# Performance work log

Hardware: AMD Instinct MI355X
Metric: run time of the kernel (lower is better)

Reference implementation:

```python
import jax, jax.numpy as jnp
import numpy as np

EMB_DIM = 128
WEIGHT_COL = 24

def setup_inputs() -> dict:
    key = jax.random.key(0)
    ks = jax.random.split(key, 9)
    B, S = 8, 4096
    s_in = 1.0 / np.sqrt(EMB_DIM)
    s_out = 1.0 / np.sqrt(WEIGHT_COL)
    return {
        "x": jax.random.normal(ks[0], (B, S, EMB_DIM), dtype=jnp.float32),
        "wQ": jax.random.uniform(ks[1], (EMB_DIM, WEIGHT_COL), jnp.float32, -s_in, s_in),
        "bQ": jax.random.uniform(ks[2], (WEIGHT_COL,), jnp.float32, -s_in, s_in),
        "wK": jax.random.uniform(ks[3], (EMB_DIM, WEIGHT_COL), jnp.float32, -s_in, s_in),
        "bK": jax.random.uniform(ks[4], (WEIGHT_COL,), jnp.float32, -s_in, s_in),
        "wV": jax.random.uniform(ks[5], (EMB_DIM, WEIGHT_COL), jnp.float32, -s_in, s_in),
        "bV": jax.random.uniform(ks[6], (WEIGHT_COL,), jnp.float32, -s_in, s_in),
        "wO": jax.random.uniform(ks[7], (WEIGHT_COL, EMB_DIM), jnp.float32, -s_out, s_out),
        "bO": jax.random.uniform(ks[8], (EMB_DIM,), jnp.float32, -s_out, s_out),
    }

def reference(x, wQ, bQ, wK, bK, wV, bV, wO, bO):
    # projections: [B,S,E] -> [B,S,D]
    Q = x @ wQ + bQ
    K = x @ wK + bK
    V = x @ wV + bV
    # NOTE: source scales by sqrt(emb_dim), not sqrt(weight_col)
    scale = 1.0 / np.sqrt(EMB_DIM).astype(np.float32)
    scores = jnp.einsum('bqd,bkd->bqk', Q, K) * scale  # [B,S,S]
    A = jax.nn.softmax(scores, axis=-1)
    H = jnp.einsum('bqk,bkd->bqd', A, V)               # [B,S,D]
    return H @ wO + bO                                  # [B,S,E]
```

## Files before the change

kernel.cpp:

```cpp
#include <hip/hip_runtime.h>


#define B_ 8
#define S_ 4096
#define E_ 128
#define D_ 24
#define N_ (B_ * S_)
#define SCALE 0.08838834764831845f
#define LOG2E 1.4426950408889634f

#define TK 128
#define KS_STRIDE 40
#define VS_STRIDE 136
#define HS_STRIDE 40
#define XS_STRIDE 136
#define OS_STRIDE 84

typedef __attribute__((ext_vector_type(8))) short bfrag;
typedef __attribute__((ext_vector_type(4))) float ffrag;

__device__ inline unsigned short f2bf(float f) {
    unsigned int x = __builtin_bit_cast(unsigned int, f);
    return (unsigned short)((x + 0x7fffu + ((x >> 16) & 1u)) >> 16);
}
__device__ inline unsigned int pack2(float a, float b) {
    return (unsigned int)f2bf(a) | ((unsigned int)f2bf(b) << 16);
}
__device__ inline unsigned int pack2h(float a, float b) {
    unsigned int ua = __builtin_bit_cast(unsigned int, a) + 0x8000u;
    unsigned int ub = __builtin_bit_cast(unsigned int, b) + 0x8000u;
    return __builtin_amdgcn_perm(ub, ua, 0x07060302);
}

__global__ __launch_bounds__(256) void prep_kernel(
    const float* __restrict__ wQ, const float* __restrict__ bQ,
    const float* __restrict__ wK, const float* __restrict__ bK,
    const float* __restrict__ wV, const float* __restrict__ bV,
    const float* __restrict__ wO,
    unsigned short* __restrict__ Wf, unsigned short* __restrict__ wOf,
    float* __restrict__ bqkv)
{
    const int gtid   = blockIdx.x * 256 + threadIdx.x;
    const int stride = gridDim.x * 256;
    const float qs = SCALE * LOG2E;
    for (int idx = gtid; idx < 4 * 5 * 512; idx += stride) {
        const int j    = idx & 7;
        const int lane = (idx >> 3) & 63;
        const int nt   = (idx >> 9) % 5;
        const int kt   = idx / 2560;
        const int n = nt * 16 + (lane & 15);
        const int k = kt * 32 + ((lane >> 4) << 3) + j;
        float v = 0.0f;
        if (n < 24)      v = wQ[k * 24 + n] * qs;
        else if (n < 48) v = wK[k * 24 + (n - 24)];
        else if (n < 72) v = wV[k * 24 + (n - 48)];
        Wf[idx] = f2bf(v);
    }
    for (int idx = gtid; idx < 8 * 512; idx += stride) {
        const int j    = idx & 7;
        const int lane = (idx >> 3) & 63;
        const int nt   = idx >> 9;
        const int k = ((lane >> 4) << 3) + j;
        const int e = nt * 16 + (lane & 15);
        wOf[idx] = (k < 24) ? f2bf(wO[k * 128 + e]) : (unsigned short)0;
    }
    if (gtid < 80) {
        float v = 0.0f;
        if (gtid < 24)      v = bQ[gtid] * qs;
        else if (gtid < 48) v = bK[gtid - 24];
        else if (gtid < 72) v = bV[gtid - 48];
        bqkv[gtid] = v;
    }
}

__global__ __launch_bounds__(256) void proj_kernel(
    const float* __restrict__ x, const unsigned short* __restrict__ Wf,
    const float* __restrict__ bqkv,
    unsigned short* __restrict__ Qbf, unsigned short* __restrict__ Kbf,
    unsigned short* __restrict__ Vt)
{
    __shared__ float smem[64 * OS_STRIDE];
    unsigned short* xs = (unsigned short*)smem;
    float* os = smem;

    const int tid  = threadIdx.x;
    const int lane = tid & 63;
    const int w    = tid >> 6;
    const int col  = lane & 15;
    const int quad = lane >> 4;
    const int rb   = blockIdx.x * 64;

    #pragma unroll
    for (int i = 0; i < 8; ++i) {
        const int idx = i * 256 + tid;
        const int row = idx >> 5, c4 = idx & 31;
        const float4 xv = *(const float4*)(x + (size_t)(rb + row) * 128 + c4 * 4);
        uint2 h;
        h.x = pack2(xv.x, xv.y);
        h.y = pack2(xv.z, xv.w);
        *(uint2*)(&xs[row * XS_STRIDE + c4 * 4]) = h;
    }

    bfrag Wfr[20];
    #pragma unroll
    for (int f = 0; f < 20; ++f)
        Wfr[f] = *(const bfrag*)(Wf + (f * 64 + lane) * 8);

    __syncthreads();

    ffrag acc[5];
    #pragma unroll
    for (int nt = 0; nt < 5; ++nt) acc[nt] = (ffrag){0.f, 0.f, 0.f, 0.f};

    #pragma unroll
    for (int kt = 0; kt < 4; ++kt) {
        const bfrag Af = *(const bfrag*)(&xs[(w * 16 + col) * XS_STRIDE + kt * 32 + quad * 8]);
        #pragma unroll
        for (int nt = 0; nt < 5; ++nt)
            acc[nt] = __builtin_amdgcn_mfma_f32_16x16x32_bf16(Af, Wfr[kt * 5 + nt], acc[nt], 0, 0, 0);
    }

    __syncthreads();

    #pragma unroll
    for (int nt = 0; nt < 5; ++nt) {
        const float bb = bqkv[nt * 16 + col];
        #pragma unroll
        for (int r = 0; r < 4; ++r)
            os[(w * 16 + quad * 4 + r) * OS_STRIDE + nt * 16 + col] = acc[nt][r] + bb;
    }
    __syncthreads();

    {
        const int half  = tid & 1;
        const int row   = (tid >> 1) & 63;
        const int isK   = tid >> 7;
        const int cbase = isK * 24;
        unsigned int pk[8];
        #pragma unroll
        for (int g = 0; g < 8; ++g) {
            const int c0 = half * 16 + g * 2;
            const float f0 = (c0     < 24) ? os[row * OS_STRIDE + cbase + c0]     : 0.0f;
            const float f1 = (c0 + 1 < 24) ? os[row * OS_STRIDE + cbase + c0 + 1] : 0.0f;
            pk[g] = pack2(f0, f1);
        }
        unsigned short* dst = (isK ? Kbf : Qbf) + (size_t)(rb + row) * 32 + half * 16;
        *(uint4*)(dst)     = make_uint4(pk[0], pk[1], pk[2], pk[3]);
        *(uint4*)(dst + 8) = make_uint4(pk[4], pk[5], pk[6], pk[7]);
    }

    if (tid < 192) {
        const int d  = tid % 24;
        const int ch = tid / 24;
        unsigned int p[4];
        #pragma unroll
        for (int g = 0; g < 4; ++g) {
            const float f0 = os[(ch * 8 + g * 2 + 0) * OS_STRIDE + 48 + d];
            const float f1 = os[(ch * 8 + g * 2 + 1) * OS_STRIDE + 48 + d];
            p[g] = pack2(f0, f1);
        }
        const int b = rb >> 12, s0 = rb & 4095;
        uint4* dst = (uint4*)(Vt + (((size_t)(b * 24 + d)) << 12) + s0 + ch * 8);
        *dst = make_uint4(p[0], p[1], p[2], p[3]);
    }
}

__global__ __launch_bounds__(256, 8) void attn_kernel(
    const unsigned short* __restrict__ Qbf, const unsigned short* __restrict__ Kbf,
    const unsigned short* __restrict__ Vt,
    float* __restrict__ Opart, float* __restrict__ lpart)
{
    __shared__ unsigned short Ks[TK * KS_STRIDE];
    __shared__ unsigned short Vs[32 * VS_STRIDE];

    const int tid    = threadIdx.x;
    const int lane   = tid & 63;
    const int w      = tid >> 6;
    const int col    = lane & 15;
    const int quad   = lane >> 4;
    const int blk    = blockIdx.x;
    const int split  = blockIdx.y;
    const int nsp    = gridDim.y;
    const int kchunk = S_ / nsp;
    const int b      = blk >> 6;
    const int qbase  = blk * 64 + w * 16;

    if (tid < 16)
        *(uint4*)(&Vs[24 * VS_STRIDE + tid * 8]) =
            make_uint4(0x3F803F80u, 0x3F803F80u, 0x3F803F80u, 0x3F803F80u);

    const bfrag Qf = *(const bfrag*)(Qbf + (size_t)(qbase + col) * 32 + quad * 8);

    ffrag Ot0 = {0.f, 0.f, 0.f, 0.f};
    ffrag Ot1 = {0.f, 0.f, 0.f, 0.f};

    const unsigned short* Kbase = Kbf + ((size_t)(b * 4096) + split * kchunk) * 32;
    const unsigned short* Vbase = Vt + (size_t)(b * 24) * 4096 + split * kchunk;

    __syncthreads();

    for (int kb = 0; kb < kchunk; kb += TK) {
        #pragma unroll
        for (int i = 0; i < 2; ++i) {
            const int idx = i * 256 + tid;
            const int key = idx >> 2, ch = idx & 3;
            const uint4 t4 = *(const uint4*)(Kbase + (size_t)(kb + key) * 32 + ch * 8);
            const int row = (key & ~31) + (((key >> 2) & 1) << 4)
                          + (((key & 31) >> 3) << 2) + (key & 3);
            *(uint4*)(&Ks[row * KS_STRIDE + ch * 8]) = t4;
        }
        #pragma unroll
        for (int i = 0; i < 2; ++i) {
            const int u = i * 256 + tid;
            if (u < 384) {
                const int d = u >> 4, ch = u & 15;
                const uint4 t4 = *(const uint4*)(Vbase + (size_t)d * 4096 + kb + ch * 8);
                *(uint4*)(&Vs[d * VS_STRIDE + ch * 8]) = t4;
            }
        }
        __syncthreads();

        #pragma unroll
        for (int c2 = 0; c2 < 4; ++c2) {
            const bfrag Kfe = *(const bfrag*)(&Ks[(c2 * 32 + col) * KS_STRIDE + quad * 8]);
            const bfrag Kfo = *(const bfrag*)(&Ks[(c2 * 32 + 16 + col) * KS_STRIDE + quad * 8]);
            ffrag Se = {0.f, 0.f, 0.f, 0.f};
            ffrag So = {0.f, 0.f, 0.f, 0.f};
            Se = __builtin_amdgcn_mfma_f32_16x16x32_bf16(Kfe, Qf, Se, 0, 0, 0);
            So = __builtin_amdgcn_mfma_f32_16x16x32_bf16(Kfo, Qf, So, 0, 0, 0);
            const float pe0 = __builtin_amdgcn_exp2f(Se[0]);
            const float pe1 = __builtin_amdgcn_exp2f(Se[1]);
            const float pe2 = __builtin_amdgcn_exp2f(Se[2]);
            const float pe3 = __builtin_amdgcn_exp2f(Se[3]);
            const float po0 = __builtin_amdgcn_exp2f(So[0]);
            const float po1 = __builtin_amdgcn_exp2f(So[1]);
            const float po2 = __builtin_amdgcn_exp2f(So[2]);
            const float po3 = __builtin_amdgcn_exp2f(So[3]);
            union { bfrag f; unsigned int u[4]; } P;
            P.u[0] = pack2h(pe0, pe1);
            P.u[1] = pack2h(pe2, pe3);
            P.u[2] = pack2h(po0, po1);
            P.u[3] = pack2h(po2, po3);
            const bfrag Va0 = *(const bfrag*)(&Vs[col * VS_STRIDE + c2 * 32 + quad * 8]);
            const bfrag Va1 = *(const bfrag*)(&Vs[(16 + col) * VS_STRIDE + c2 * 32 + quad * 8]);
            Ot0 = __builtin_amdgcn_mfma_f32_16x16x32_bf16(Va0, P.f, Ot0, 0, 0, 0);
            Ot1 = __builtin_amdgcn_mfma_f32_16x16x32_bf16(Va1, P.f, Ot1, 0, 0, 0);
        }
        __syncthreads();
    }

    const size_t base = ((size_t)split * N_ + qbase + col) * 32;
    *(ffrag*)(&Opart[base + quad * 4]) = Ot0;
    if (quad < 2)
        *(ffrag*)(&Opart[base + 16 + quad * 4]) = Ot1;
    if (quad == 2)
        lpart[(size_t)split * N_ + qbase + col] = Ot1[0];
}

__global__ __launch_bounds__(256) void combine_kernel(
    const float* __restrict__ Opart, const float* __restrict__ lpart,
    const unsigned short* __restrict__ wOf, const float* __restrict__ bO,
    float* __restrict__ out, int nsp)
{
    __shared__ unsigned short Hs[64 * HS_STRIDE];

    const int tid = threadIdx.x;
    const int qb  = blockIdx.x * 64;
    {
        const int ql = tid >> 2;
        const int c8 = (tid & 3) * 8;
        const int q  = qb + ql;
        float a[8] = {0.f, 0.f, 0.f, 0.f, 0.f, 0.f, 0.f, 0.f};
        if (c8 < 24) {
            for (int s = 0; s < nsp; ++s) {
                const float* p = &Opart[((size_t)s * N_ + q) * 32 + c8];
                const float4 u = *(const float4*)p;
                const float4 v = *(const float4*)(p + 4);
                a[0] += u.x; a[1] += u.y; a[2] += u.z; a[3] += u.w;
                a[4] += v.x; a[5] += v.y; a[6] += v.z; a[7] += v.w;
            }
        }
        float ls = 0.f;
        for (int s = 0; s < nsp; ++s) ls += lpart[(size_t)s * N_ + q];
        const float inv = 1.0f / ls;
        uint4 pk;
        pk.x = pack2(a[0] * inv, a[1] * inv);
        pk.y = pack2(a[2] * inv, a[3] * inv);
        pk.z = pack2(a[4] * inv, a[5] * inv);
        pk.w = pack2(a[6] * inv, a[7] * inv);
        *(uint4*)(&Hs[ql * HS_STRIDE + c8]) = pk;
    }
    __syncthreads();

    const int lane = tid & 63;
    const int w    = tid >> 6;
    const int col  = lane & 15;
    const int quad = lane >> 4;
    const bfrag Hf = *(const bfrag*)(&Hs[(w * 16 + col) * HS_STRIDE + quad * 8]);
    #pragma unroll
    for (int nt = 0; nt < 8; ++nt) {
        const bfrag Wo = *(const bfrag*)(wOf + (nt * 64 + lane) * 8);
        ffrag C = {0.f, 0.f, 0.f, 0.f};
        C = __builtin_amdgcn_mfma_f32_16x16x32_bf16(Hf, Wo, C, 0, 0, 0);
        const float bo = bO[nt * 16 + col];
        #pragma unroll
        for (int r = 0; r < 4; ++r)
            out[(size_t)(qb + w * 16 + quad * 4 + r) * 128 + nt * 16 + col] = C[r] + bo;
    }
}

extern "C" void kernel_launch(void* const* d_in, const int* in_sizes, int n_in,
                              void* d_out, int out_size, void* d_ws, size_t ws_size,
                              hipStream_t stream) {
    const float* x  = (const float*)d_in[0];
    const float* wQ = (const float*)d_in[1];
    const float* bQ = (const float*)d_in[2];
    const float* wK = (const float*)d_in[3];
    const float* bK = (const float*)d_in[4];
    const float* wV = (const float*)d_in[5];
    const float* bV = (const float*)d_in[6];
    const float* wO = (const float*)d_in[7];
    const float* bO = (const float*)d_in[8];
    float* out = (float*)d_out;

    unsigned short* ws16 = (unsigned short*)d_ws;
    unsigned short* Qbf = ws16;
    unsigned short* Kbf = Qbf + (size_t)N_ * 32;
    unsigned short* Vt  = Kbf + (size_t)N_ * 32;
    unsigned short* Wf  = Vt + (size_t)B_ * 24 * S_;
    unsigned short* wOf = Wf + 4 * 5 * 512;
    float* bqkv = (float*)(wOf + 8 * 512);
    float* Opart = bqkv + 80;
    const size_t baseBytes = (size_t)((char*)Opart - (char*)d_ws);

    int nsp = 4;
    while (nsp > 1) {
        const size_t need = baseBytes + (size_t)nsp * N_ * 32 * 4 + (size_t)nsp * N_ * 4;
        if (need <= ws_size) break;
        nsp >>= 1;
    }
    float* lpart = Opart + (size_t)nsp * N_ * 32;

    prep_kernel<<<8, 256, 0, stream>>>(wQ, bQ, wK, bK, wV, bV, wO, Wf, wOf, bqkv);
    proj_kernel<<<N_ / 64, 256, 0, stream>>>(x, Wf, bqkv, Qbf, Kbf, Vt);
    attn_kernel<<<dim3(N_ / 64, nsp), 256, 0, stream>>>(Qbf, Kbf, Vt, Opart, lpart);
    combine_kernel<<<N_ / 64, 256, 0, stream>>>(Opart, lpart, wOf, bO, out, nsp);
}
```

Before: 125.1 us.

## Process two query tiles per wave in attention kernel to reuse K/V tiles

Each wave now handles two 16-row query tiles (128 queries per block instead of 64), so every K and V fragment loaded from shared memory feeds twice as many MFMAs. The grid halves and launch bounds drop to 4 blocks per CU to allow for the doubled accumulator and score registers. This cuts the global-to-LDS staging of K/V per query and the LDS fragment reads, but lowers occupancy and halves the number of blocks available to spread across CUs.

```diff
diff --git a/kernel.cpp b/kernel.cpp
--- a/kernel.cpp
+++ b/kernel.cpp
@@ -165,7 +165,7 @@
     }
 }
 
-__global__ __launch_bounds__(256, 8) void attn_kernel(
+__global__ __launch_bounds__(256, 4) void attn_kernel(
     const unsigned short* __restrict__ Qbf, const unsigned short* __restrict__ Kbf,
     const unsigned short* __restrict__ Vt,
     float* __restrict__ Opart, float* __restrict__ lpart)
@@ -182,17 +182,21 @@
     const int split  = blockIdx.y;
     const int nsp    = gridDim.y;
     const int kchunk = S_ / nsp;
-    const int b      = blk >> 6;
-    const int qbase  = blk * 64 + w * 16;
+    const int b      = blk >> 5;
+    const int qbase0 = blk * 128 + w * 16;
+    const int qbase1 = qbase0 + 64;
 
     if (tid < 16)
         *(uint4*)(&Vs[24 * VS_STRIDE + tid * 8]) =
             make_uint4(0x3F803F80u, 0x3F803F80u, 0x3F803F80u, 0x3F803F80u);
 
-    const bfrag Qf = *(const bfrag*)(Qbf + (size_t)(qbase + col) * 32 + quad * 8);
-
-    ffrag Ot0 = {0.f, 0.f, 0.f, 0.f};
-    ffrag Ot1 = {0.f, 0.f, 0.f, 0.f};
+    const bfrag Qf0 = *(const bfrag*)(Qbf + (size_t)(qbase0 + col) * 32 + quad * 8);
+    const bfrag Qf1 = *(const bfrag*)(Qbf + (size_t)(qbase1 + col) * 32 + quad * 8);
+
+    ffrag Ot00 = {0.f, 0.f, 0.f, 0.f};
+    ffrag Ot10 = {0.f, 0.f, 0.f, 0.f};
+    ffrag Ot01 = {0.f, 0.f, 0.f, 0.f};
+    ffrag Ot11 = {0.f, 0.f, 0.f, 0.f};
 
     const unsigned short* Kbase = Kbf + ((size_t)(b * 4096) + split * kchunk) * 32;
     const unsigned short* Vbase = Vt + (size_t)(b * 24) * 4096 + split * kchunk;
@@ -224,37 +228,47 @@
         for (int c2 = 0; c2 < 4; ++c2) {
             const bfrag Kfe = *(const bfrag*)(&Ks[(c2 * 32 + col) * KS_STRIDE + quad * 8]);
             const bfrag Kfo = *(const bfrag*)(&Ks[(c2 * 32 + 16 + col) * KS_STRIDE + quad * 8]);
-            ffrag Se = {0.f, 0.f, 0.f, 0.f};
-            ffrag So = {0.f, 0.f, 0.f, 0.f};
-            Se = __builtin_amdgcn_mfma_f32_16x16x32_bf16(Kfe, Qf, Se, 0, 0, 0);
-            So = __builtin_amdgcn_mfma_f32_16x16x32_bf16(Kfo, Qf, So, 0, 0, 0);
-            const float pe0 = __builtin_amdgcn_exp2f(Se[0]);
-            const float pe1 = __builtin_amdgcn_exp2f(Se[1]);
-            const float pe2 = __builtin_amdgcn_exp2f(Se[2]);
-            const float pe3 = __builtin_amdgcn_exp2f(Se[3]);
-            const float po0 = __builtin_amdgcn_exp2f(So[0]);
-            const float po1 = __builtin_amdgcn_exp2f(So[1]);
-            const float po2 = __builtin_amdgcn_exp2f(So[2]);
-            const float po3 = __builtin_amdgcn_exp2f(So[3]);
-            union { bfrag f; unsigned int u[4]; } P;
-            P.u[0] = pack2h(pe0, pe1);
-            P.u[1] = pack2h(pe2, pe3);
-            P.u[2] = pack2h(po0, po1);
-            P.u[3] = pack2h(po2, po3);
+            ffrag Se0 = {0.f, 0.f, 0.f, 0.f};
+            ffrag So0 = {0.f, 0.f, 0.f, 0.f};
+            ffrag Se1 = {0.f, 0.f, 0.f, 0.f};
+            ffrag So1 = {0.f, 0.f, 0.f, 0.f};
+            Se0 = __builtin_amdgcn_mfma_f32_16x16x32_bf16(Kfe, Qf0, Se0, 0, 0, 0);
+            So0 = __builtin_amdgcn_mfma_f32_16x16x32_bf16(Kfo, Qf0, So0, 0, 0, 0);
+            Se1 = __builtin_amdgcn_mfma_f32_16x16x32_bf16(Kfe, Qf1, Se1, 0, 0, 0);
+            So1 = __builtin_amdgcn_mfma_f32_16x16x32_bf16(Kfo, Qf1, So1, 0, 0, 0);
+
+            union { bfrag f; unsigned int u[4]; } P0, P1;
+            P0.u[0] = pack2h(__builtin_amdgcn_exp2f(Se0[0]), __builtin_amdgcn_exp2f(Se0[1]));
+            P0.u[1] = pack2h(__builtin_amdgcn_exp2f(Se0[2]), __builtin_amdgcn_exp2f(Se0[3]));
+            P0.u[2] = pack2h(__builtin_amdgcn_exp2f(So0[0]), __builtin_amdgcn_exp2f(So0[1]));
+            P0.u[3] = pack2h(__builtin_amdgcn_exp2f(So0[2]), __builtin_amdgcn_exp2f(So0[3]));
+            P1.u[0] = pack2h(__builtin_amdgcn_exp2f(Se1[0]), __builtin_amdgcn_exp2f(Se1[1]));
+            P1.u[1] = pack2h(__builtin_amdgcn_exp2f(Se1[2]), __builtin_amdgcn_exp2f(Se1[3]));
+            P1.u[2] = pack2h(__builtin_amdgcn_exp2f(So1[0]), __builtin_amdgcn_exp2f(So1[1]));
+            P1.u[3] = pack2h(__builtin_amdgcn_exp2f(So1[2]), __builtin_amdgcn_exp2f(So1[3]));
+
             const bfrag Va0 = *(const bfrag*)(&Vs[col * VS_STRIDE + c2 * 32 + quad * 8]);
             const bfrag Va1 = *(const bfrag*)(&Vs[(16 + col) * VS_STRIDE + c2 * 32 + quad * 8]);
-            Ot0 = __builtin_amdgcn_mfma_f32_16x16x32_bf16(Va0, P.f, Ot0, 0, 0, 0);
-            Ot1 = __builtin_amdgcn_mfma_f32_16x16x32_bf16(Va1, P.f, Ot1, 0, 0, 0);
+            Ot00 = __builtin_amdgcn_mfma_f32_16x16x32_bf16(Va0, P0.f, Ot00, 0, 0, 0);
+            Ot10 = __builtin_amdgcn_mfma_f32_16x16x32_bf16(Va1, P0.f, Ot10, 0, 0, 0);
+            Ot01 = __builtin_amdgcn_mfma_f32_16x16x32_bf16(Va0, P1.f, Ot01, 0, 0, 0);
+            Ot11 = __builtin_amdgcn_mfma_f32_16x16x32_bf16(Va1, P1.f, Ot11, 0, 0, 0);
         }
         __syncthreads();
     }
 
-    const size_t base = ((size_t)split * N_ + qbase + col) * 32;
-    *(ffrag*)(&Opart[base + quad * 4]) = Ot0;
-    if (quad < 2)
-        *(ffrag*)(&Opart[base + 16 + quad * 4]) = Ot1;
-    if (quad == 2)
-        lpart[(size_t)split * N_ + qbase + col] = Ot1[0];
+    const size_t base0 = ((size_t)split * N_ + qbase0 + col) * 32;
+    const size_t base1 = ((size_t)split * N_ + qbase1 + col) * 32;
+    *(ffrag*)(&Opart[base0 + quad * 4]) = Ot00;
+    *(ffrag*)(&Opart[base1 + quad * 4]) = Ot01;
+    if (quad < 2) {
+        *(ffrag*)(&Opart[base0 + 16 + quad * 4]) = Ot10;
+        *(ffrag*)(&Opart[base1 + 16 + quad * 4]) = Ot11;
+    }
+    if (quad == 2) {
+        lpart[(size_t)split * N_ + qbase0 + col] = Ot10[0];
+        lpart[(size_t)split * N_ + qbase1 + col] = Ot11[0];
+    }
 }
 
 __global__ __launch_bounds__(256) void combine_kernel(
@@ -343,6 +357,6 @@
 
     prep_kernel<<<8, 256, 0, stream>>>(wQ, bQ, wK, bK, wV, bV, wO, Wf, wOf, bqkv);
     proj_kernel<<<N_ / 64, 256, 0, stream>>>(x, Wf, bqkv, Qbf, Kbf, Vt);
-    attn_kernel<<<dim3(N_ / 64, nsp), 256, 0, stream>>>(Qbf, Kbf, Vt, Opart, lpart);
+    attn_kernel<<<dim3(N_ / 128, nsp), 256, 0, stream>>>(Qbf, Kbf, Vt, Opart, lpart);
     combine_kernel<<<N_ / 64, 256, 0, stream>>>(Opart, lpart, wOf, bO, out, nsp);
 }
```

Result: no change. 125.2 us (+0.1%).

## Use 512-thread attention blocks, fp16 partial outputs, and cheaper bf16 packing

Applied to the files above, without the earlier changes.

Attention blocks now have 512 threads covering 128 queries, so each K/V tile staged in shared memory serves twice as many query rows. The partial output accumulators go to the workspace as fp16 instead of fp32, which halves the write and read traffic between the attention and combine kernels. The round-to-nearest-even bf16 packing is replaced by the cheaper add-and-permute packing in the projection and combine kernels. Risks are lower precision in the partial outputs, a possible fp16 overflow on large unnormalized sums, and reduced occupancy from the larger blocks.

```diff
diff --git a/kernel.cpp b/kernel.cpp
--- a/kernel.cpp
+++ b/kernel.cpp
@@ -1,4 +1,5 @@
 #include <hip/hip_runtime.h>
+#include <hip/hip_fp16.h>
 
 
 #define B_ 8
@@ -23,13 +24,13 @@
     unsigned int x = __builtin_bit_cast(unsigned int, f);
     return (unsigned short)((x + 0x7fffu + ((x >> 16) & 1u)) >> 16);
 }
-__device__ inline unsigned int pack2(float a, float b) {
-    return (unsigned int)f2bf(a) | ((unsigned int)f2bf(b) << 16);
-}
 __device__ inline unsigned int pack2h(float a, float b) {
     unsigned int ua = __builtin_bit_cast(unsigned int, a) + 0x8000u;
     unsigned int ub = __builtin_bit_cast(unsigned int, b) + 0x8000u;
     return __builtin_amdgcn_perm(ub, ua, 0x07060302);
+}
+__device__ inline unsigned int packh16(float a, float b) {
+    return __builtin_bit_cast(unsigned int, __builtin_amdgcn_cvt_pkrtz(a, b));
 }
 
 __global__ __launch_bounds__(256) void prep_kernel(
@@ -96,8 +97,8 @@
         const int row = idx >> 5, c4 = idx & 31;
         const float4 xv = *(const float4*)(x + (size_t)(rb + row) * 128 + c4 * 4);
         uint2 h;
-        h.x = pack2(xv.x, xv.y);
-        h.y = pack2(xv.z, xv.w);
+        h.x = pack2h(xv.x, xv.y);
+        h.y = pack2h(xv.z, xv.w);
         *(uint2*)(&xs[row * XS_STRIDE + c4 * 4]) = h;
     }
 
@@ -142,7 +143,7 @@
             const int c0 = half * 16 + g * 2;
             const float f0 = (c0     < 24) ? os[row * OS_STRIDE + cbase + c0]     : 0.0f;
             const float f1 = (c0 + 1 < 24) ? os[row * OS_STRIDE + cbase + c0 + 1] : 0.0f;
-            pk[g] = pack2(f0, f1);
+            pk[g] = pack2h(f0, f1);
         }
         unsigned short* dst = (isK ? Kbf : Qbf) + (size_t)(rb + row) * 32 + half * 16;
         *(uint4*)(dst)     = make_uint4(pk[0], pk[1], pk[2], pk[3]);
@@ -157,7 +158,7 @@
         for (int g = 0; g < 4; ++g) {
             const float f0 = os[(ch * 8 + g * 2 + 0) * OS_STRIDE + 48 + d];
             const float f1 = os[(ch * 8 + g * 2 + 1) * OS_STRIDE + 48 + d];
-            p[g] = pack2(f0, f1);
+            p[g] = pack2h(f0, f1);
         }
         const int b = rb >> 12, s0 = rb & 4095;
         uint4* dst = (uint4*)(Vt + (((size_t)(b * 24 + d)) << 12) + s0 + ch * 8);
@@ -165,10 +166,10 @@
     }
 }
 
-__global__ __launch_bounds__(256, 8) void attn_kernel(
+__global__ __launch_bounds__(512, 8) void attn_kernel(
     const unsigned short* __restrict__ Qbf, const unsigned short* __restrict__ Kbf,
     const unsigned short* __restrict__ Vt,
-    float* __restrict__ Opart, float* __restrict__ lpart)
+    __half* __restrict__ Opart, float* __restrict__ lpart)
 {
     __shared__ unsigned short Ks[TK * KS_STRIDE];
     __shared__ unsigned short Vs[32 * VS_STRIDE];
@@ -182,8 +183,8 @@
     const int split  = blockIdx.y;
     const int nsp    = gridDim.y;
     const int kchunk = S_ / nsp;
-    const int b      = blk >> 6;
-    const int qbase  = blk * 64 + w * 16;
+    const int b      = blk >> 5;
+    const int qbase  = blk * 128 + w * 16;
 
     if (tid < 16)
         *(uint4*)(&Vs[24 * VS_STRIDE + tid * 8]) =
@@ -200,23 +201,17 @@
     __syncthreads();
 
     for (int kb = 0; kb < kchunk; kb += TK) {
-        #pragma unroll
-        for (int i = 0; i < 2; ++i) {
-            const int idx = i * 256 + tid;
-            const int key = idx >> 2, ch = idx & 3;
+        {
+            const int key = tid >> 2, ch = tid & 3;
             const uint4 t4 = *(const uint4*)(Kbase + (size_t)(kb + key) * 32 + ch * 8);
             const int row = (key & ~31) + (((key >> 2) & 1) << 4)
                           + (((key & 31) >> 3) << 2) + (key & 3);
             *(uint4*)(&Ks[row * KS_STRIDE + ch * 8]) = t4;
         }
-        #pragma unroll
-        for (int i = 0; i < 2; ++i) {
-            const int u = i * 256 + tid;
-            if (u < 384) {
-                const int d = u >> 4, ch = u & 15;
-                const uint4 t4 = *(const uint4*)(Vbase + (size_t)d * 4096 + kb + ch * 8);
-                *(uint4*)(&Vs[d * VS_STRIDE + ch * 8]) = t4;
-            }
+        if (tid < 384) {
+            const int d = tid >> 4, ch = tid & 15;
+            const uint4 t4 = *(const uint4*)(Vbase + (size_t)d * 4096 + kb + ch * 8);
+            *(uint4*)(&Vs[d * VS_STRIDE + ch * 8]) = t4;
         }
         __syncthreads();
 
@@ -228,19 +223,11 @@
             ffrag So = {0.f, 0.f, 0.f, 0.f};
             Se = __builtin_amdgcn_mfma_f32_16x16x32_bf16(Kfe, Qf, Se, 0, 0, 0);
             So = __builtin_amdgcn_mfma_f32_16x16x32_bf16(Kfo, Qf, So, 0, 0, 0);
-            const float pe0 = __builtin_amdgcn_exp2f(Se[0]);
-            const float pe1 = __builtin_amdgcn_exp2f(Se[1]);
-            const float pe2 = __builtin_amdgcn_exp2f(Se[2]);
-            const float pe3 = __builtin_amdgcn_exp2f(Se[3]);
-            const float po0 = __builtin_amdgcn_exp2f(So[0]);
-            const float po1 = __builtin_amdgcn_exp2f(So[1]);
-            const float po2 = __builtin_amdgcn_exp2f(So[2]);
-            const float po3 = __builtin_amdgcn_exp2f(So[3]);
             union { bfrag f; unsigned int u[4]; } P;
-            P.u[0] = pack2h(pe0, pe1);
-            P.u[1] = pack2h(pe2, pe3);
-            P.u[2] = pack2h(po0, po1);
-            P.u[3] = pack2h(po2, po3);
+            P.u[0] = pack2h(__builtin_amdgcn_exp2f(Se[0]), __builtin_amdgcn_exp2f(Se[1]));
+            P.u[1] = pack2h(__builtin_amdgcn_exp2f(Se[2]), __builtin_amdgcn_exp2f(Se[3]));
+            P.u[2] = pack2h(__builtin_amdgcn_exp2f(So[0]), __builtin_amdgcn_exp2f(So[1]));
+            P.u[3] = pack2h(__builtin_amdgcn_exp2f(So[2]), __builtin_amdgcn_exp2f(So[3]));
             const bfrag Va0 = *(const bfrag*)(&Vs[col * VS_STRIDE + c2 * 32 + quad * 8]);
             const bfrag Va1 = *(const bfrag*)(&Vs[(16 + col) * VS_STRIDE + c2 * 32 + quad * 8]);
             Ot0 = __builtin_amdgcn_mfma_f32_16x16x32_bf16(Va0, P.f, Ot0, 0, 0, 0);
@@ -250,15 +237,24 @@
     }
 
     const size_t base = ((size_t)split * N_ + qbase + col) * 32;
-    *(ffrag*)(&Opart[base + quad * 4]) = Ot0;
-    if (quad < 2)
-        *(ffrag*)(&Opart[base + 16 + quad * 4]) = Ot1;
+    {
+        uint2 s0;
+        s0.x = packh16(Ot0[0], Ot0[1]);
+        s0.y = packh16(Ot0[2], Ot0[3]);
+        *(uint2*)(Opart + base + quad * 4) = s0;
+    }
+    if (quad < 2) {
+        uint2 s1;
+        s1.x = packh16(Ot1[0], Ot1[1]);
+        s1.y = packh16(Ot1[2], Ot1[3]);
+        *(uint2*)(Opart + base + 16 + quad * 4) = s1;
+    }
     if (quad == 2)
         lpart[(size_t)split * N_ + qbase + col] = Ot1[0];
 }
 
 __global__ __launch_bounds__(256) void combine_kernel(
-    const float* __restrict__ Opart, const float* __restrict__ lpart,
+    const __half* __restrict__ Opart, const float* __restrict__ lpart,
     const unsigned short* __restrict__ wOf, const float* __restrict__ bO,
     float* __restrict__ out, int nsp)
 {
@@ -273,21 +269,23 @@
         float a[8] = {0.f, 0.f, 0.f, 0.f, 0.f, 0.f, 0.f, 0.f};
         if (c8 < 24) {
             for (int s = 0; s < nsp; ++s) {
-                const float* p = &Opart[((size_t)s * N_ + q) * 32 + c8];
-                const float4 u = *(const float4*)p;
-                const float4 v = *(const float4*)(p + 4);
-                a[0] += u.x; a[1] += u.y; a[2] += u.z; a[3] += u.w;
-                a[4] += v.x; a[5] += v.y; a[6] += v.z; a[7] += v.w;
+                const __half2* p2 = (const __half2*)(Opart + ((size_t)s * N_ + q) * 32 + c8);
+                #pragma unroll
+                for (int j = 0; j < 4; ++j) {
+                    const float2 f = __half22float2(p2[j]);
+                    a[2 * j]     += f.x;
+                    a[2 * j + 1] += f.y;
+                }
             }
         }
         float ls = 0.f;
         for (int s = 0; s < nsp; ++s) ls += lpart[(size_t)s * N_ + q];
         const float inv = 1.0f / ls;
         uint4 pk;
-        pk.x = pack2(a[0] * inv, a[1] * inv);
-        pk.y = pack2(a[2] * inv, a[3] * inv);
-        pk.z = pack2(a[4] * inv, a[5] * inv);
-        pk.w = pack2(a[6] * inv, a[7] * inv);
+        pk.x = pack2h(a[0] * inv, a[1] * inv);
+        pk.y = pack2h(a[2] * inv, a[3] * inv);
+        pk.z = pack2h(a[4] * inv, a[5] * inv);
+        pk.w = pack2h(a[6] * inv, a[7] * inv);
         *(uint4*)(&Hs[ql * HS_STRIDE + c8]) = pk;
     }
     __syncthreads();
@@ -330,19 +328,19 @@
     unsigned short* Wf  = Vt + (size_t)B_ * 24 * S_;
     unsigned short* wOf = Wf + 4 * 5 * 512;
     float* bqkv = (float*)(wOf + 8 * 512);
-    float* Opart = bqkv + 80;
+    __half* Opart = (__half*)(bqkv + 80);
     const size_t baseBytes = (size_t)((char*)Opart - (char*)d_ws);
 
     int nsp = 4;
     while (nsp > 1) {
-        const size_t need = baseBytes + (size_t)nsp * N_ * 32 * 4 + (size_t)nsp * N_ * 4;
+        const size_t need = baseBytes + (size_t)nsp * N_ * 32 * 2 + (size_t)nsp * N_ * 4;
         if (need <= ws_size) break;
         nsp >>= 1;
     }
-    float* lpart = Opart + (size_t)nsp * N_ * 32;
+    float* lpart = (float*)(Opart + (size_t)nsp * N_ * 32);
 
     prep_kernel<<<8, 256, 0, stream>>>(wQ, bQ, wK, bK, wV, bV, wO, Wf, wOf, bqkv);
     proj_kernel<<<N_ / 64, 256, 0, stream>>>(x, Wf, bqkv, Qbf, Kbf, Vt);
-    attn_kernel<<<dim3(N_ / 64, nsp), 256, 0, stream>>>(Qbf, Kbf, Vt, Opart, lpart);
+    attn_kernel<<<dim3(N_ / 128, nsp), 512, 0, stream>>>(Qbf, Kbf, Vt, Opart, lpart);
     combine_kernel<<<N_ / 64, 256, 0, stream>>>(Opart, lpart, wOf, bO, out, nsp);
 }
```

After: 122.3 us. 2.3% less time.
